# Performance work log

Measured on AMD Instinct MI355X. Metric: run time of the kernel, lower is better.

The kernel has to match this reference:

```python
import jax, jax.numpy as jnp
import numpy as np

DIM = 2048
NUM_HEADS = 16
NUM_KV_HEADS = 4
HEAD_DIM = DIM // NUM_HEADS  # 128
ROPE_BASE = 10000.0
BATCH = 2
SEQLEN = 2048


def _rms_norm(x):
    # F.rms_norm over last dim, no weight; torch default eps = dtype eps
    eps = jnp.finfo(x.dtype).eps
    ms = jnp.mean(jnp.square(x), axis=-1, keepdims=True)
    return x * jax.lax.rsqrt(ms + eps)


def _rotary_cos_sin(seqlen, dtype):
    # Rotary(head_dim, base): inv_freq over even indices, freqs = t outer inv_freq
    inv_freq = 1.0 / (ROPE_BASE ** (jnp.arange(0, HEAD_DIM, 2, dtype=jnp.float32) / HEAD_DIM))
    t = jnp.arange(seqlen, dtype=jnp.float32)
    freqs = jnp.outer(t, inv_freq)  # [T, HEAD_DIM//2]
    return jnp.cos(freqs).astype(dtype), jnp.sin(freqs).astype(dtype)


def _apply_rotary_emb(x, cos, sin):
    # x: [B, H, T, D]; split halves (modded-nanogpt style)
    d = x.shape[-1] // 2
    x1, x2 = x[..., :d], x[..., d:]
    y1 = x1 * cos + x2 * sin
    y2 = -x1 * sin + x2 * cos
    return jnp.concatenate([y1, y2], axis=-1)


def setup_inputs() -> dict:
    key = jax.random.key(0)
    ks = jax.random.split(key, 6)
    kv_dim = NUM_KV_HEADS * HEAD_DIM
    s_in = 1.0 / np.sqrt(DIM)
    return {
        "x": jax.random.normal(ks[0], (BATCH, SEQLEN, DIM), dtype=jnp.float32),
        "q_gain": jax.random.uniform(ks[1], (NUM_HEADS,), dtype=jnp.float32, minval=0.5, maxval=1.5),
        "W_q": jax.random.normal(ks[2], (DIM, DIM), dtype=jnp.float32) * s_in,
        "W_k": jax.random.normal(ks[3], (kv_dim, DIM), dtype=jnp.float32) * s_in,
        "W_v": jax.random.normal(ks[4], (kv_dim, DIM), dtype=jnp.float32) * s_in,
        "W_proj": jax.random.normal(ks[5], (DIM, DIM), dtype=jnp.float32) * s_in,
    }


def reference(x, q_gain, W_q, W_k, W_v, W_proj):
    B, T, D = x.shape
    # QKV projections (Linear with weight [out, in])
    q = (x @ W_q.T).reshape(B, T, NUM_HEADS, HEAD_DIM).transpose(0, 2, 1, 3)   # [B,H,T,d]
    k = (x @ W_k.T).reshape(B, T, NUM_KV_HEADS, HEAD_DIM).transpose(0, 2, 1, 3)
    v = (x @ W_v.T).reshape(B, T, NUM_KV_HEADS, HEAD_DIM).transpose(0, 2, 1, 3)
    # dual RMSNorm on q/k
    q = _rms_norm(q)
    k = _rms_norm(k)
    # RoPE
    cos, sin = _rotary_cos_sin(T, q.dtype)
    q = _apply_rotary_emb(q, cos, sin)
    k = _apply_rotary_emb(k, cos, sin)
    # per-head gain on q
    q = q * q_gain.astype(q.dtype)[None, :, None, None]
    # GQA: repeat kv heads to match query heads
    g = NUM_HEADS // NUM_KV_HEADS
    k = jnp.repeat(k, g, axis=1)
    v = jnp.repeat(v, g, axis=1)
    # causal scaled dot product attention
    scale = 1.0 / np.sqrt(HEAD_DIM)
    scores = jnp.einsum('bhqd,bhkd->bhqk', q, k) * scale
    causal = jnp.tril(jnp.ones((T, T), dtype=bool))
    scores = jnp.where(causal[None, None], scores, jnp.finfo(scores.dtype).min)
    probs = jax.nn.softmax(scores, axis=-1)
    y = jnp.einsum('bhqk,bhkd->bhqd', probs, v)  # [B,H,T,d]
    y = y.transpose(0, 2, 1, 3).reshape(B, T, D)
    return y @ W_proj.T
```

## Files before the change

### kernel.cpp

```cpp
#include <hip/hip_runtime.h>
#include <hip/hip_bf16.h>
#include <type_traits>

#define DIMN   2048
#define NH     16
#define NKVH   4
#define HD     128
#define KVD    512
#define NQKV   3072
#define BATCH  2
#define SEQ    2048
#define MROWS  4096
#define VOFF   2560

typedef __attribute__((ext_vector_type(8))) __bf16 bf16x8;
typedef __attribute__((ext_vector_type(4))) float floatx4;

#define BIG_NEG (-1.0e30f)

__device__ __forceinline__ short bf16rn(float f) {
  union { float f; unsigned u; } v; v.f = f;
  unsigned u = v.u;
  return (short)((u + 0x7fffu + ((u >> 16) & 1u)) >> 16);
}
__device__ __forceinline__ float bf2f(short s) {
  union { unsigned u; float f; } v;
  v.u = ((unsigned)(unsigned short)s) << 16;
  return v.f;
}

__device__ __forceinline__ void async_cp16(const short* g, short* l) {
  __builtin_amdgcn_global_load_lds(
      (const __attribute__((address_space(1))) unsigned int*)g,
      (__attribute__((address_space(3))) unsigned int*)l, 16, 0, 0);
}

__global__ void f32_to_bf16_kern(const float* __restrict__ in,
                                 short* __restrict__ out, int n8) {
  int i = blockIdx.x * blockDim.x + threadIdx.x;
  if (i >= n8) return;
  float4 a = ((const float4*)in)[i * 2];
  float4 b = ((const float4*)in)[i * 2 + 1];
  short r[8];
  r[0] = bf16rn(a.x); r[1] = bf16rn(a.y); r[2] = bf16rn(a.z); r[3] = bf16rn(a.w);
  r[4] = bf16rn(b.x); r[5] = bf16rn(b.y); r[6] = bf16rn(b.z); r[7] = bf16rn(b.w);
  ((uint4*)out)[i] = *(const uint4*)r;
}

template <typename OUT>
__global__ __launch_bounds__(256) void gemm_bt_as(const short* __restrict__ A,
                                                  const short* __restrict__ Bw,
                                                  OUT* __restrict__ C,
                                                  int N, int K) {
  __shared__ __align__(16) short As[2][128 * 32];
  __shared__ __align__(16) short Bs[2][128 * 32];
  const int t = threadIdx.x;
  const int lane = t & 63, wave = t >> 6;
  const int lrow = lane & 15, quad = lane >> 4;
  const int wr = wave >> 1, wc = wave & 1;
  const int m0 = blockIdx.y * 128, n0 = blockIdx.x * 128;

  const short* pa[2];
  const short* pb[2];
  int wi2[2];
#pragma unroll
  for (int i = 0; i < 2; i++) {
    int wi = wave * 2 + i;
    int row = wi * 16 + (lane >> 2);
    int col = ((lane & 3) ^ (row & 3)) * 8;
    pa[i] = A + (size_t)(m0 + row) * K + col;
    pb[i] = Bw + (size_t)(n0 + row) * K + col;
    wi2[i] = wi;
  }

  floatx4 acc[4][4] = {};
  const int iters = K >> 5;

#pragma unroll
  for (int i = 0; i < 2; i++) {
    async_cp16(pa[i], &As[0][wi2[i] * 512]);
    async_cp16(pb[i], &Bs[0][wi2[i] * 512]);
  }

  for (int it = 0; it < iters; it++) {
    const int cur = it & 1;
    __syncthreads();

    if (it + 1 < iters) {
      const int off = (it + 1) * 32;
#pragma unroll
      for (int i = 0; i < 2; i++) {
        async_cp16(pa[i] + off, &As[cur ^ 1][wi2[i] * 512]);
        async_cp16(pb[i] + off, &Bs[cur ^ 1][wi2[i] * 512]);
      }
    }

    bf16x8 af[4], bfr[4];
#pragma unroll
    for (int mt = 0; mt < 4; mt++) {
      int row = wr * 64 + mt * 16 + lrow;
      af[mt] = *(const bf16x8*)&As[cur][row * 32 + (quad ^ (lrow & 3)) * 8];
    }
#pragma unroll
    for (int nt = 0; nt < 4; nt++) {
      int row = wc * 64 + nt * 16 + lrow;
      bfr[nt] = *(const bf16x8*)&Bs[cur][row * 32 + (quad ^ (lrow & 3)) * 8];
    }
#pragma unroll
    for (int mt = 0; mt < 4; mt++)
#pragma unroll
      for (int nt = 0; nt < 4; nt++)
        acc[mt][nt] = __builtin_amdgcn_mfma_f32_16x16x32_bf16(af[mt], bfr[nt],
                                                              acc[mt][nt], 0, 0, 0);
  }

#pragma unroll
  for (int mt = 0; mt < 4; mt++)
#pragma unroll
    for (int nt = 0; nt < 4; nt++) {
      int row = m0 + wr * 64 + mt * 16 + quad * 4;
      int col = n0 + wc * 64 + nt * 16 + lrow;
#pragma unroll
      for (int r = 0; r < 4; r++) {
        if constexpr (std::is_same<OUT, short>::value)
          C[(size_t)(row + r) * N + col] = bf16rn(acc[mt][nt][r]);
        else
          C[(size_t)(row + r) * N + col] = acc[mt][nt][r];
      }
    }
}

__global__ __launch_bounds__(256) void rms_rope_kern(const short* __restrict__ qkv,
                                                     const float* __restrict__ gain,
                                                     short* __restrict__ qb,
                                                     short* __restrict__ kb) {
  const int t = threadIdx.x;
  const int lane = t & 63, wave = t >> 6;
  const int gw = blockIdx.x * 4 + wave;
  const int row = gw / 20, slot = gw - row * 20;
  const int pos = row & (SEQ - 1);

  const short* src = (slot < 16) ? qkv + (size_t)row * NQKV + slot * HD
                                 : qkv + (size_t)row * NQKV + DIMN + (slot - 16) * HD;
  float x1 = bf2f(src[lane]), x2 = bf2f(src[lane + 64]);

  float ss = x1 * x1 + x2 * x2;
#pragma unroll
  for (int off = 32; off > 0; off >>= 1) ss += __shfl_xor(ss, off);
  float inv = rsqrtf(ss * (1.0f / 128.0f) + 1.1920928955078125e-7f);
  x1 *= inv; x2 *= inv;
  float fr = (float)pos * exp2f((float)lane * -0.20762050593045935f);
  float s, c;
  sincosf(fr, &s, &c);
  float y1 = x1 * c + x2 * s;
  float y2 = x2 * c - x1 * s;
  if (slot < 16) {
    float g = gain[slot] * 0.12751744459132754f;
    y1 *= g; y2 *= g;
  }
  short o1 = bf16rn(y1), o2 = bf16rn(y2);
  if (slot < 16) { short* d = qb + (size_t)row * DIMN + slot * HD;        d[lane] = o1; d[lane + 64] = o2; }
  else           { short* d = kb + (size_t)row * KVD + (slot - 16) * HD;  d[lane] = o1; d[lane + 64] = o2; }
}

__global__ __launch_bounds__(256) void vT_kern(const short* __restrict__ qkv,
                                               short* __restrict__ vT) {
  __shared__ short L[64 * 68];
  const int t0 = blockIdx.x * 64, d0 = blockIdx.y * 64;
  const int b = blockIdx.z >> 2, kvh = blockIdx.z & 3;
  const int t = threadIdx.x;

#pragma unroll
  for (int p = 0; p < 4; p++) {
    int tt = p * 16 + (t >> 4);
    int dd = (t & 15) * 4;
    ushort4 v = *(const ushort4*)(qkv + (size_t)(b * SEQ + t0 + tt) * NQKV + VOFF + kvh * HD + d0 + dd);
    *(ushort4*)&L[tt * 68 + dd] = v;
  }
  __syncthreads();

  const int dl = t >> 2;
  const int tc = (t & 3) * 16;
  short tmp[16];
#pragma unroll
  for (int j = 0; j < 16; j++) tmp[j] = L[(tc + j) * 68 + dl];
  size_t obase = (size_t)((b * NKVH + kvh) * HD + d0 + dl) * SEQ + t0 + tc;
  *(uint4*)(vT + obase)     = ((const uint4*)tmp)[0];
  *(uint4*)(vT + obase + 8) = ((const uint4*)tmp)[1];
}

__global__ __launch_bounds__(256) void attn_kern(const short* __restrict__ qb,
                                                 const short* __restrict__ kb,
                                                 const short* __restrict__ vT,
                                                 short* __restrict__ yb) {
  __shared__ __align__(16) short Ks[2][64 * 128];
  __shared__ __align__(16) short Vs[128 * 64];
  __shared__ __align__(16) short Ps[64 * 72];
  const int qp = blockIdx.x;
  const int g  = blockIdx.y;
  const int b = g >> 4, h = g & 15, kvh = h >> 2;
  const int t = threadIdx.x, lane = t & 63, wave = t >> 6;
  const int lrow = lane & 15, quad = lane >> 4;

  int k_row[4], k_col[4], v_row[4], v_col[4];
#pragma unroll
  for (int i = 0; i < 4; i++) {
    int wi = wave * 4 + i;
    int kr = wi * 4 + (lane >> 4);
    k_row[i] = kr; k_col[i] = ((lane & 15) ^ (kr & 7)) * 8;
    int vr = wi * 8 + (lane >> 3);
    v_row[i] = vr; v_col[i] = ((lane & 7) ^ (vr & 7)) * 8;
  }
  const short* kbase = kb + (size_t)b * SEQ * KVD + kvh * HD;
  const short* vbase = vT + (size_t)(b * NKVH + kvh) * HD * SEQ;

  for (int ph = 0; ph < 2; ph++) {
    const int qt = ph ? (31 - qp) : qp;
    const int q0 = qt * 64;

    __syncthreads();

    bf16x8 aq[4];
    const short* qrow = qb + (size_t)(b * SEQ + q0 + wave * 16 + lrow) * DIMN + h * HD;
#pragma unroll
    for (int kk = 0; kk < 4; kk++)
      aq[kk] = *(const bf16x8*)(qrow + kk * 32 + quad * 8);

    floatx4 O[8] = {};
    float mI[4], lI[4];
#pragma unroll
    for (int r = 0; r < 4; r++) { mI[r] = BIG_NEG; lI[r] = 0.0f; }

#pragma unroll
    for (int i = 0; i < 4; i++)
      async_cp16(kbase + (size_t)k_row[i] * KVD + k_col[i], &Ks[0][(wave * 4 + i) * 512]);

    for (int kt = 0; kt <= qt; kt++) {
      const int cur = kt & 1;
      const int k0 = kt * 64;
      __syncthreads();

#pragma unroll
      for (int i = 0; i < 4; i++)
        async_cp16(vbase + (size_t)v_row[i] * SEQ + k0 + v_col[i], &Vs[(wave * 4 + i) * 512]);
      if (kt < qt) {
        const int kn = k0 + 64;
#pragma unroll
        for (int i = 0; i < 4; i++)
          async_cp16(kbase + (size_t)(kn + k_row[i]) * KVD + k_col[i],
                     &Ks[cur ^ 1][(wave * 4 + i) * 512]);
      }

      floatx4 S[4] = {};
#pragma unroll
      for (int kk = 0; kk < 4; kk++)
#pragma unroll
        for (int nt = 0; nt < 4; nt++) {
          int row = nt * 16 + lrow;
          bf16x8 bk = *(const bf16x8*)&Ks[cur][row * 128 + ((kk * 4 + quad) ^ (row & 7)) * 8];
          S[nt] = __builtin_amdgcn_mfma_f32_16x16x32_bf16(aq[kk], bk, S[nt], 0, 0, 0);
        }

      if (kt == qt) {
#pragma unroll
        for (int nt = 0; nt < 4; nt++) {
          int kj = nt * 16 + lrow;
#pragma unroll
          for (int r = 0; r < 4; r++) {
            int qi = wave * 16 + quad * 4 + r;
            if (kj > qi) S[nt][r] = BIG_NEG;
          }
        }
      }

#pragma unroll
      for (int r = 0; r < 4; r++) {
        float mx = fmaxf(fmaxf(S[0][r], S[1][r]), fmaxf(S[2][r], S[3][r]));
        mx = fmaxf(mx, __shfl_xor(mx, 1));
        mx = fmaxf(mx, __shfl_xor(mx, 2));
        mx = fmaxf(mx, __shfl_xor(mx, 4));
        mx = fmaxf(mx, __shfl_xor(mx, 8));
        float mNew = fmaxf(mI[r], mx);
        float alpha = exp2f(mI[r] - mNew);
        float ssum = 0.0f;
#pragma unroll
        for (int nt = 0; nt < 4; nt++) {
          float p = exp2f(S[nt][r] - mNew);
          S[nt][r] = p;
          ssum += p;
        }
        ssum += __shfl_xor(ssum, 1);
        ssum += __shfl_xor(ssum, 2);
        ssum += __shfl_xor(ssum, 4);
        ssum += __shfl_xor(ssum, 8);
        lI[r] = lI[r] * alpha + ssum;
        mI[r] = mNew;
#pragma unroll
        for (int n2 = 0; n2 < 8; n2++) O[n2][r] *= alpha;
      }

#pragma unroll
      for (int nt = 0; nt < 4; nt++) {
        int cwr = ((nt * 2 + (lrow >> 3)) ^ (quad * 2)) * 8 + (lrow & 7);
#pragma unroll
        for (int r = 0; r < 4; r++)
          Ps[(wave * 16 + quad * 4 + r) * 72 + cwr] = bf16rn(S[nt][r]);
      }

      __syncthreads();

#pragma unroll
      for (int kk = 0; kk < 2; kk++) {
        int capc = ((kk * 4 + quad) ^ (2 * ((lrow >> 2) & 3))) * 8;
        bf16x8 ap = *(const bf16x8*)&Ps[(wave * 16 + lrow) * 72 + capc];
#pragma unroll
        for (int n2 = 0; n2 < 8; n2++) {
          int row = n2 * 16 + lrow;
          bf16x8 bv = *(const bf16x8*)&Vs[row * 64 + ((kk * 4 + quad) ^ (row & 7)) * 8];
          O[n2] = __builtin_amdgcn_mfma_f32_16x16x32_bf16(ap, bv, O[n2], 0, 0, 0);
        }
      }
    }

#pragma unroll
    for (int n2 = 0; n2 < 8; n2++)
#pragma unroll
      for (int r = 0; r < 4; r++) {
        float val = O[n2][r] / lI[r];
        int row = q0 + wave * 16 + quad * 4 + r;
        int col = h * HD + n2 * 16 + lrow;
        yb[(size_t)(b * SEQ + row) * DIMN + col] = bf16rn(val);
      }
  }
}

extern "C" void kernel_launch(void* const* d_in, const int* in_sizes, int n_in,
                              void* d_out, int out_size, void* d_ws, size_t ws_size,
                              hipStream_t stream) {
  const float* x      = (const float*)d_in[0];
  const float* q_gain = (const float*)d_in[1];
  const float* W_q    = (const float*)d_in[2];
  const float* W_k    = (const float*)d_in[3];
  const float* W_v    = (const float*)d_in[4];
  const float* W_proj = (const float*)d_in[5];
  float* out = (float*)d_out;
  char* ws = (char*)d_ws;

  short* xb    = (short*)(ws);
  short* wqkv  = (short*)(ws + 16777216);
  short* wproj = (short*)(ws + 29360128);
  short* qkvb  = (short*)(ws + 37748736);
  short* q     = (short*)(ws + 62914560);
  short* k     = (short*)(ws + 79691776);
  short* vT    = (short*)(ws + 83886080);
  short* y     = xb;

  auto cvt = [&](const float* src, short* dst, int n) {
    int n8 = n / 8;
    f32_to_bf16_kern<<<(n8 + 255) / 256, 256, 0, stream>>>(src, dst, n8);
  };
  cvt(x, xb, MROWS * DIMN);
  cvt(W_q, wqkv, DIMN * DIMN);
  cvt(W_k, wqkv + DIMN * DIMN, KVD * DIMN);
  cvt(W_v, wqkv + DIMN * DIMN + KVD * DIMN, KVD * DIMN);
  cvt(W_proj, wproj, DIMN * DIMN);

  gemm_bt_as<short><<<dim3(NQKV / 128, MROWS / 128), 256, 0, stream>>>(xb, wqkv, qkvb, NQKV, DIMN);
  rms_rope_kern<<<(MROWS * 20) / 4, 256, 0, stream>>>(qkvb, q_gain, q, k);
  vT_kern<<<dim3(SEQ / 64, HD / 64, BATCH * NKVH), 256, 0, stream>>>(qkvb, vT);
  attn_kern<<<dim3(16, 32), 256, 0, stream>>>(q, k, vT, y);
  gemm_bt_as<float><<<dim3(DIMN / 128, MROWS / 128), 256, 0, stream>>>(y, wproj, out, DIMN, DIMN);
}
```

Measured before the change: 348.5 us.

## Compute softmax row sums via MFMA and skip rescaling with lazy max update

Flash-attention's online softmax now updates the running max and rescales the accumulators only when some row's new max exceeds the old one by more than a threshold, checked wave-uniformly. The per-row shuffle reductions of exp sums are replaced by an extra MFMA of the probability tile against a ones vector, so the denominator accumulates alongside O. The bf16 conversion uses the native cast, and the final normalization multiplies by a reciprocal instead of dividing. This cuts VALU and cross-lane shuffle work in the inner loop. In exchange it adds one MFMA per k-step, and the denominator is summed from bf16-rounded probabilities, with exp values allowed up to 2^8 before a rescale.

```diff
diff --git a/kernel.cpp b/kernel.cpp
--- a/kernel.cpp
+++ b/kernel.cpp
@@ -19,9 +19,9 @@
 #define BIG_NEG (-1.0e30f)
 
 __device__ __forceinline__ short bf16rn(float f) {
-  union { float f; unsigned u; } v; v.f = f;
-  unsigned u = v.u;
-  return (short)((u + 0x7fffu + ((u >> 16) & 1u)) >> 16);
+  union { __bf16 h; short s; } u;
+  u.h = (__bf16)f;
+  return u.s;
 }
 __device__ __forceinline__ float bf2f(short s) {
   union { unsigned u; float f; } v;
@@ -214,6 +214,10 @@
   const short* kbase = kb + (size_t)b * SEQ * KVD + kvh * HD;
   const short* vbase = vT + (size_t)(b * NKVH + kvh) * HD * SEQ;
 
+  bf16x8 vones;
+#pragma unroll
+  for (int j = 0; j < 8; j++) vones[j] = (__bf16)1.0f;
+
   for (int ph = 0; ph < 2; ph++) {
     const int qt = ph ? (31 - qp) : qp;
     const int q0 = qt * 64;
@@ -227,9 +231,10 @@
       aq[kk] = *(const bf16x8*)(qrow + kk * 32 + quad * 8);
 
     floatx4 O[8] = {};
-    float mI[4], lI[4];
-#pragma unroll
-    for (int r = 0; r < 4; r++) { mI[r] = BIG_NEG; lI[r] = 0.0f; }
+    floatx4 Ol = {};
+    float mI[4];
+#pragma unroll
+    for (int r = 0; r < 4; r++) mI[r] = BIG_NEG;
 
 #pragma unroll
     for (int i = 0; i < 4; i++)
@@ -280,23 +285,16 @@
         mx = fmaxf(mx, __shfl_xor(mx, 2));
         mx = fmaxf(mx, __shfl_xor(mx, 4));
         mx = fmaxf(mx, __shfl_xor(mx, 8));
-        float mNew = fmaxf(mI[r], mx);
-        float alpha = exp2f(mI[r] - mNew);
-        float ssum = 0.0f;
-#pragma unroll
-        for (int nt = 0; nt < 4; nt++) {
-          float p = exp2f(S[nt][r] - mNew);
-          S[nt][r] = p;
-          ssum += p;
+        if (!__all(mx <= mI[r] + 8.0f)) {
+          float mNew = fmaxf(mI[r], mx);
+          float alpha = exp2f(mI[r] - mNew);
+          mI[r] = mNew;
+#pragma unroll
+          for (int n2 = 0; n2 < 8; n2++) O[n2][r] *= alpha;
+          Ol[r] *= alpha;
         }
-        ssum += __shfl_xor(ssum, 1);
-        ssum += __shfl_xor(ssum, 2);
-        ssum += __shfl_xor(ssum, 4);
-        ssum += __shfl_xor(ssum, 8);
-        lI[r] = lI[r] * alpha + ssum;
-        mI[r] = mNew;
-#pragma unroll
-        for (int n2 = 0; n2 < 8; n2++) O[n2][r] *= alpha;
+#pragma unroll
+        for (int nt = 0; nt < 4; nt++) S[nt][r] = exp2f(S[nt][r] - mI[r]);
       }
 
 #pragma unroll
@@ -319,14 +317,18 @@
           bf16x8 bv = *(const bf16x8*)&Vs[row * 64 + ((kk * 4 + quad) ^ (row & 7)) * 8];
           O[n2] = __builtin_amdgcn_mfma_f32_16x16x32_bf16(ap, bv, O[n2], 0, 0, 0);
         }
-      }
-    }
-
+        Ol = __builtin_amdgcn_mfma_f32_16x16x32_bf16(ap, vones, Ol, 0, 0, 0);
+      }
+    }
+
+    float il[4];
+#pragma unroll
+    for (int r = 0; r < 4; r++) il[r] = 1.0f / Ol[r];
 #pragma unroll
     for (int n2 = 0; n2 < 8; n2++)
 #pragma unroll
       for (int r = 0; r < 4; r++) {
-        float val = O[n2][r] / lI[r];
+        float val = O[n2][r] * il[r];
         int row = q0 + wave * 16 + quad * 4 + r;
         int col = h * HD + n2 * 16 + lrow;
         yb[(size_t)(b * SEQ + row) * DIMN + col] = bf16rn(val);
```

Result: no change. 353.0 us (+1.3%).
